# Kernel optimization log

Measured on AMD Instinct MI355X. Metric: run time of the kernel, lower is better.

The kernel has to match this reference:

```python
import jax, jax.numpy as jnp
import numpy as np

B, S, D = 2, 2048, 1024
H, DH = 16, 64
LN_EPS = 1e-5
NEG_INF = -1e9


def setup_inputs() -> dict:
    key = jax.random.key(0)
    ks = jax.random.split(key, 8)
    x = jax.random.normal(ks[0], (B, S, D), dtype=jnp.float32)
    mask = jax.random.randint(ks[1], (B, 1, S, S), 0, 5) == 0
    sc = 1.0 / np.sqrt(D)
    W_attn = jax.random.normal(ks[2], (D, 3 * H * DH), dtype=jnp.float32) * sc
    b_attn = jnp.zeros((3 * H * DH,), dtype=jnp.float32)
    W_out = jax.random.normal(ks[3], (H * DH, D), dtype=jnp.float32) * sc
    b_out = jnp.zeros((D,), dtype=jnp.float32)
    ln_g = jnp.ones((D,), dtype=jnp.float32)
    ln_b = jnp.zeros((D,), dtype=jnp.float32)
    return {"x": x, "W_attn": W_attn, "b_attn": b_attn, "W_out": W_out,
            "b_out": b_out, "ln_g": ln_g, "ln_b": ln_b, "mask": mask}


def reference(x, W_attn, b_attn, W_out, b_out, ln_g, ln_b, mask):
    bs, s, _ = x.shape
    qkv = x @ W_attn + b_attn                      # [b, s, 3*H*DH]
    q, k, v = jnp.split(qkv, 3, axis=-1)
    q = q.reshape(bs, s, H, DH)
    k = k.reshape(bs, s, H, DH)
    v = v.reshape(bs, s, H, DH)
    scores = jnp.einsum('bqhd,bkhd->bhqk', q, k) / np.sqrt(DH)
    scores = jnp.where(mask, NEG_INF, scores)
    probs = jax.nn.softmax(scores, axis=-1)        # attn_p = 0 -> dropout is identity
    attn = jnp.einsum('bhqk,bkhd->bqhd', probs, v).reshape(bs, s, H * DH)
    y = x + (attn @ W_out + b_out)                 # resid_p = 0
    mu = jnp.mean(y, axis=-1, keepdims=True)
    var = jnp.mean((y - mu) ** 2, axis=-1, keepdims=True)
    return (y - mu) * jax.lax.rsqrt(var + LN_EPS) * ln_g + ln_b
```

## Files before the change

kernel.cpp:

```cpp
#include <hip/hip_runtime.h>
#include <math.h>

#define BB 2
#define SS 2048
#define DD 1024
#define HH 16
#define DHD 64
#define N3 3072
#define LN_EPS 1e-5f

#define PLANE (BB*HH*SS*DHD)

typedef __attribute__((ext_vector_type(8))) short bf16x8;
typedef __attribute__((ext_vector_type(4))) float f32x4;
typedef __attribute__((ext_vector_type(16))) float f32x16;
typedef unsigned int u32;
typedef unsigned short ushort_t;

static __device__ __forceinline__ short f2bf(float f) {
  union { float f; unsigned u; } a;
  a.f = f;
  unsigned r = a.u + 0x7fffu + ((a.u >> 16) & 1u);
  return (short)(r >> 16);
}

static __device__ __forceinline__ u32 fbits(float f) {
  union { float f; u32 u; } a; a.f = f; return a.u;
}

static __device__ __forceinline__ float ex2(float x) {
  float r;
  asm("v_exp_f32 %0, %1" : "=v"(r) : "v"(x));
  return r;
}

static __device__ __forceinline__ u32 pkbf(float lo, float hi) {
  return __builtin_amdgcn_perm(fbits(hi) + 0x8000u, fbits(lo) + 0x8000u,
                               0x07060302u);
}

static __device__ __forceinline__ void gload_lds16(const void* g, void* l) {
  __builtin_amdgcn_global_load_lds(
      (const __attribute__((address_space(1))) u32*)g,
      (__attribute__((address_space(3))) u32*)l, 16, 0, 0);
}

#define PREP_CONV_B   2048
#define PREP_TA_B     768
#define PREP_TO_B     256
#define PREP_PACK_B   32768
#define PREP_TOTAL_B  (PREP_CONV_B + PREP_TA_B + PREP_TO_B + PREP_PACK_B)

__global__ __launch_bounds__(256) void prep_kernel(
    const float* __restrict__ x, ushort_t* __restrict__ xb,
    const float* __restrict__ Wa, ushort_t* __restrict__ watt,
    const float* __restrict__ Wo, ushort_t* __restrict__ wot,
    const int* __restrict__ mask, unsigned long long* __restrict__ bits) {
  __shared__ float tile[64][65];
  const int tid = threadIdx.x;
  const int bid = blockIdx.x;

  if (bid < PREP_CONV_B) {
    int i = (bid * 256 + tid) * 8;
    float4 a = *(const float4*)&x[i];
    float4 b = *(const float4*)&x[i + 4];
    short s[8] = {f2bf(a.x), f2bf(a.y), f2bf(a.z), f2bf(a.w),
                  f2bf(b.x), f2bf(b.y), f2bf(b.z), f2bf(b.w)};
    *(bf16x8*)&xb[i] = *(bf16x8*)s;
    return;
  }
  if (bid < PREP_CONV_B + PREP_TA_B + PREP_TO_B) {
    const float* W; ushort_t* Wt; int K, N, nb, kb;
    if (bid < PREP_CONV_B + PREP_TA_B) {
      int idx = bid - PREP_CONV_B;
      W = Wa; Wt = watt; K = DD; N = N3;
      nb = (idx % 48) * 64; kb = (idx / 48) * 64;
    } else {
      int idx = bid - PREP_CONV_B - PREP_TA_B;
      W = Wo; Wt = wot; K = DD; N = DD;
      nb = (idx % 16) * 64; kb = (idx / 16) * 64;
    }
    #pragma unroll
    for (int i = 0; i < 4; ++i) {
      int idx = tid + i * 256;
      int r = idx >> 4, c = (idx & 15) * 4;
      float4 v = *(const float4*)&W[(size_t)(kb + r) * N + nb + c];
      tile[r][c] = v.x; tile[r][c + 1] = v.y;
      tile[r][c + 2] = v.z; tile[r][c + 3] = v.w;
    }
    __syncthreads();
    #pragma unroll
    for (int i = 0; i < 4; ++i) {
      int idx = tid + i * 256;
      int n = idx >> 4, k = (idx & 15) * 4;
      short4 s;
      s.x = f2bf(tile[k][n]); s.y = f2bf(tile[k + 1][n]);
      s.z = f2bf(tile[k + 2][n]); s.w = f2bf(tile[k + 3][n]);
      *(short4*)&Wt[(size_t)(nb + n) * K + kb + k] = s;
    }
    return;
  }
  {
    size_t g = (size_t)(bid - PREP_CONV_B - PREP_TA_B - PREP_TO_B) * 256 + tid;
    int m = mask[g];
    unsigned long long b = __ballot(m != 0);
    if ((tid & 63) == 0) bits[g >> 6] = b;
  }
}

#define GEMM_MAIN(Aptr, Btptr, Kdim)                                          \
  __shared__ ushort_t As[128 * 64];                                           \
  __shared__ ushort_t Bs[128 * 64];                                           \
  const int tid = threadIdx.x;                                                \
  const int wave = tid >> 6, lane = tid & 63;                                 \
  const int lane16 = lane & 15, quad = lane >> 4;                             \
  const int wm = wave & 1, wn = wave >> 1;                                    \
  const int bm = blockIdx.y * 128, bn = blockIdx.x * 128;                     \
  const int srow = lane >> 3;                                                 \
  const int sg = (lane & 7) ^ srow;                                           \
  f32x4 acc[4][4];                                                            \
  _Pragma("unroll") for (int i = 0; i < 4; ++i)                               \
    _Pragma("unroll") for (int j = 0; j < 4; ++j)                             \
      acc[i][j] = (f32x4){0.f, 0.f, 0.f, 0.f};                                \
  const ushort_t* agp[4];                                                     \
  const ushort_t* bgp[4];                                                     \
  _Pragma("unroll") for (int i = 0; i < 4; ++i) {                             \
    int seg = wave * 4 + i;                                                   \
    int r = seg * 8 + srow;                                                   \
    agp[i] = Aptr + (size_t)(bm + r) * Kdim + sg * 8;                         \
    bgp[i] = Btptr + (size_t)(bn + r) * Kdim + sg * 8;                        \
  }                                                                           \
  for (int k0 = 0; k0 < Kdim; k0 += 64) {                                     \
    _Pragma("unroll") for (int i = 0; i < 4; ++i) {                           \
      int seg = wave * 4 + i;                                                 \
      gload_lds16(agp[i] + k0, &As[seg * 512]);                               \
      gload_lds16(bgp[i] + k0, &Bs[seg * 512]);                               \
    }                                                                         \
    __syncthreads();                                                          \
    _Pragma("unroll") for (int ks = 0; ks < 2; ++ks) {                        \
      bf16x8 af[4], bfr[4];                                                   \
      _Pragma("unroll") for (int mt = 0; mt < 4; ++mt) {                      \
        int ra = wm * 64 + mt * 16 + lane16;                                  \
        int kc = ks * 4 + quad;                                               \
        af[mt] = *(const bf16x8*)&As[ra * 64 + ((kc ^ (ra & 7)) * 8)];        \
      }                                                                       \
      _Pragma("unroll") for (int nt = 0; nt < 4; ++nt) {                      \
        int rb = wn * 64 + nt * 16 + lane16;                                  \
        int kc = ks * 4 + quad;                                               \
        bfr[nt] = *(const bf16x8*)&Bs[rb * 64 + ((kc ^ (rb & 7)) * 8)];       \
      }                                                                       \
      _Pragma("unroll") for (int mt = 0; mt < 4; ++mt)                        \
        _Pragma("unroll") for (int nt = 0; nt < 4; ++nt)                      \
          acc[mt][nt] = __builtin_amdgcn_mfma_f32_16x16x32_bf16(              \
              af[mt], bfr[nt], acc[mt][nt], 0, 0, 0);                         \
    }                                                                         \
    __syncthreads();                                                          \
  }

__global__ __launch_bounds__(256) void gemm_qkv_mfma(
    const ushort_t* __restrict__ A, const ushort_t* __restrict__ Bt,
    const float* __restrict__ bias, ushort_t* __restrict__ qkvh,
    ushort_t* __restrict__ vtb) {
  GEMM_MAIN(A, Bt, DD)
  #pragma unroll
  for (int nt = 0; nt < 4; ++nt) {
    int col = bn + wn * 64 + nt * 16 + lane16;
    int which = col >> 10, hcol = col & 1023;
    int head = hcol >> 6, d = hcol & 63;
    float bv = bias[col];
    if (which == 2) {
      #pragma unroll
      for (int mt = 0; mt < 4; ++mt) {
        #pragma unroll
        for (int reg = 0; reg < 4; ++reg) {
          int row = bm + wm * 64 + mt * 16 + quad * 4 + reg;
          int bb = row >> 11, ss = row & (SS - 1);
          vtb[((size_t)(bb * HH + head) * DHD + d) * SS + ss] =
              (ushort_t)f2bf(acc[mt][nt][reg] + bv);
        }
      }
    } else {
      ushort_t* plane = qkvh + (size_t)which * PLANE;
      #pragma unroll
      for (int mt = 0; mt < 4; ++mt) {
        #pragma unroll
        for (int reg = 0; reg < 4; ++reg) {
          int row = bm + wm * 64 + mt * 16 + quad * 4 + reg;
          int bb = row >> 11, ss = row & (SS - 1);
          plane[((size_t)(bb * HH + head) * SS + ss) * DHD + d] =
              (ushort_t)f2bf(acc[mt][nt][reg] + bv);
        }
      }
    }
  }
}

__global__ __launch_bounds__(256) void gemm_proj_mfma(
    const ushort_t* __restrict__ A, const ushort_t* __restrict__ Bt,
    const float* __restrict__ bias, const float* __restrict__ xres,
    float* __restrict__ Y) {
  GEMM_MAIN(A, Bt, DD)
  #pragma unroll
  for (int nt = 0; nt < 4; ++nt) {
    int col = bn + wn * 64 + nt * 16 + lane16;
    float bv = bias[col];
    #pragma unroll
    for (int mt = 0; mt < 4; ++mt) {
      #pragma unroll
      for (int reg = 0; reg < 4; ++reg) {
        int row = bm + wm * 64 + mt * 16 + quad * 4 + reg;
        Y[(size_t)row * DD + col] =
            acc[mt][nt][reg] + bv + xres[(size_t)row * DD + col];
      }
    }
  }
}

__global__ __launch_bounds__(512, 4) void attn_mfma_kernel(
    const ushort_t* __restrict__ qh, const ushort_t* __restrict__ kh,
    const ushort_t* __restrict__ vt, const u32* __restrict__ mbits,
    ushort_t* __restrict__ attn_out) {
  __shared__ __align__(16) ushort_t S[2][2][2][4096];

  const int tid = threadIdx.x;
  const int wave = tid >> 6, lane = tid & 63;
  const int l31 = lane & 31, hi = lane >> 5;

  const int bh = blockIdx.x & 31;
  const int qt = blockIdx.x >> 5;
  const int bbi = bh >> 4, hhi = bh & 15;
  const size_t head_base = (size_t)bh * SS * DHD;
  const int wq = wave & 3, khx = wave >> 2;
  const int q32 = qt * 128 + wq * 32;
  const int qrow = q32 + l31;

  bf16x8 qf[4];
  {
    const float kScale = 0.125f * 1.44269504f;
    const ushort_t* qsrc = &qh[head_base + (size_t)qrow * DHD + hi * 8];
    #pragma unroll
    for (int dk = 0; dk < 4; ++dk) {
      bf16x8 r = *(const bf16x8*)&qsrc[dk * 16];
      #pragma unroll
      for (int e = 0; e < 8; ++e) {
        union { u32 u; float f; } c;
        c.u = ((u32)(ushort_t)r[e]) << 16;
        c.f *= kScale;
        r[e] = f2bf(c.f);
      }
      qf[dk] = r;
    }
  }

  f32x16 acc0, acc1;
  #pragma unroll
  for (int e = 0; e < 16; ++e) { acc0[e] = 0.f; acc1[e] = 0.f; }
  float lsum = 0.f;

  const u32* mrow = mbits + ((size_t)(bbi * SS) + qrow) * 64 + khx * 32;

  const int sr = tid >> 3;
  const int scsrc = (tid & 7) ^ (sr & 7);
  const ushort_t* kst0 = kh + head_base + (size_t)sr * DHD + scsrc * 8;
  const ushort_t* vst0 = vt + head_base + (size_t)sr * SS + scsrc * 8;
  const int sdst = wave * 512;

#define ATTN_STAGE(buf, t)                                                    \
  gload_lds16(kst0 + (size_t)(t) * 64 * DHD, &S[buf][0][0][sdst]);            \
  gload_lds16(kst0 + (size_t)(1024 + (t) * 64) * DHD, &S[buf][0][1][sdst]);   \
  gload_lds16(vst0 + (t) * 64, &S[buf][1][0][sdst]);                          \
  gload_lds16(vst0 + 1024 + (t) * 64, &S[buf][1][1][sdst]);

  ATTN_STAGE(0, 0);
  uint2 mcur = *(const uint2*)mrow;
  __syncthreads();

  const int NT = 16;
  for (int t = 0; t < NT; ++t) {
    const int cur = t & 1;
    uint2 mnext = mcur;
    if (t + 1 < NT) {
      ATTN_STAGE(cur ^ 1, t + 1);
      mnext = *(const uint2*)&mrow[(t + 1) * 2];
    }

    const ushort_t* Kb = &S[cur][0][khx][0];
    const ushort_t* Vb = &S[cur][1][khx][0];

    f32x16 s0, s1;
    #pragma unroll
    for (int e = 0; e < 16; ++e) { s0[e] = 0.f; s1[e] = 0.f; }
    #pragma unroll
    for (int dk = 0; dk < 4; ++dk) {
      const int c = 2 * dk + hi;
      const int r0 = l31;
      bf16x8 kf0 = *(const bf16x8*)&Kb[r0 * 64 + ((c ^ (r0 & 7)) * 8)];
      s0 = __builtin_amdgcn_mfma_f32_32x32x16_bf16(kf0, qf[dk], s0, 0, 0, 0);
      const int r1 = 32 + l31;
      bf16x8 kf1 = *(const bf16x8*)&Kb[r1 * 64 + ((c ^ (r1 & 7)) * 8)];
      s1 = __builtin_amdgcn_mfma_f32_32x32x16_bf16(kf1, qf[dk], s1, 0, 0, 0);
    }

    #pragma unroll
    for (int ks16 = 0; ks16 < 4; ++ks16) {
      const int ksub = ks16 >> 1;
      const int g0 = (ks16 & 1) * 2;
      const f32x16 sv = ksub ? s1 : s0;
      const u32 w32 = ksub ? mcur.y : mcur.x;
      const u32 na = w32 >> (g0 * 8 + hi * 4);
      const u32 nb = w32 >> (g0 * 8 + 8 + hi * 4);
      float e0 = (na & 1u) ? 0.f : ex2(sv[g0 * 4 + 0]);
      float e1 = (na & 2u) ? 0.f : ex2(sv[g0 * 4 + 1]);
      float e2 = (na & 4u) ? 0.f : ex2(sv[g0 * 4 + 2]);
      float e3 = (na & 8u) ? 0.f : ex2(sv[g0 * 4 + 3]);
      float f0 = (nb & 1u) ? 0.f : ex2(sv[g0 * 4 + 4]);
      float f1 = (nb & 2u) ? 0.f : ex2(sv[g0 * 4 + 5]);
      float f2 = (nb & 4u) ? 0.f : ex2(sv[g0 * 4 + 6]);
      float f3 = (nb & 8u) ? 0.f : ex2(sv[g0 * 4 + 7]);
      lsum += ((e0 + e1) + (e2 + e3)) + ((f0 + f1) + (f2 + f3));
      u32 a0 = pkbf(e0, e1), a1 = pkbf(e2, e3);
      u32 b0 = pkbf(f0, f1), b1 = pkbf(f2, f3);
      asm("v_permlane32_swap_b32 %0, %1" : "+v"(a0), "+v"(b0));
      asm("v_permlane32_swap_b32 %0, %1" : "+v"(a1), "+v"(b1));
      union { u32 w[4]; bf16x8 v; } pfu;
      pfu.w[0] = a0; pfu.w[1] = a1; pfu.w[2] = b0; pfu.w[3] = b1;
      {
        const int rv0 = l31;
        const int cv = 2 * ks16 + hi;
        bf16x8 vf0 = *(const bf16x8*)&Vb[rv0 * 64 + ((cv ^ (rv0 & 7)) * 8)];
        acc0 = __builtin_amdgcn_mfma_f32_32x32x16_bf16(pfu.v, vf0, acc0, 0, 0, 0);
        const int rv1 = 32 + l31;
        bf16x8 vf1 = *(const bf16x8*)&Vb[rv1 * 64 + ((cv ^ (rv1 & 7)) * 8)];
        acc1 = __builtin_amdgcn_mfma_f32_32x32x16_bf16(pfu.v, vf1, acc1, 0, 0, 0);
      }
    }

    mcur = mnext;
    __syncthreads();
  }
#undef ATTN_STAGE

  float* mbuf = (float*)&S[0][0][0][0];
  float* lbuf = mbuf + 4 * 64 * 33;
  lbuf[((khx * 4 + wq) * 2 + hi) * 32 + l31] = lsum;
  if (khx == 1) {
    float* dst = mbuf + (size_t)(wq * 64 + lane) * 33;
    #pragma unroll
    for (int e = 0; e < 16; ++e) { dst[e] = acc0[e]; dst[16 + e] = acc1[e]; }
  }
  __syncthreads();
  if (khx == 0) {
    const float* src = mbuf + (size_t)(wq * 64 + lane) * 33;
    #pragma unroll
    for (int e = 0; e < 16; ++e) { acc0[e] += src[e]; acc1[e] += src[16 + e]; }
    #pragma unroll
    for (int reg = 0; reg < 16; ++reg) {
      const int kq = (reg & 3) + 8 * (reg >> 2) + 4 * hi;
      float lq = lbuf[((0 * 4 + wq) * 2 + 0) * 32 + kq]
               + lbuf[((0 * 4 + wq) * 2 + 1) * 32 + kq]
               + lbuf[((1 * 4 + wq) * 2 + 0) * 32 + kq]
               + lbuf[((1 * 4 + wq) * 2 + 1) * 32 + kq];
      const float inv = 1.0f / lq;
      ushort_t* orow = &attn_out[((size_t)(bbi * SS) + q32 + kq) * DD
                                 + hhi * DHD];
      orow[l31] = (ushort_t)f2bf(acc0[reg] * inv);
      orow[32 + l31] = (ushort_t)f2bf(acc1[reg] * inv);
    }
  }
}

__global__ __launch_bounds__(256) void ln_kernel(
    float* __restrict__ Y, const float* __restrict__ g,
    const float* __restrict__ bta) {
  const int r = blockIdx.x;
  const int tid = threadIdx.x;
  float4 v = *(const float4*)&Y[(size_t)r * DD + tid * 4];
  float sum = v.x + v.y + v.z + v.w;
  float sq = v.x * v.x + v.y * v.y + v.z * v.z + v.w * v.w;
  #pragma unroll
  for (int off = 32; off; off >>= 1) {
    sum += __shfl_down(sum, off);
    sq += __shfl_down(sq, off);
  }
  __shared__ float ps[4], pq[4];
  __shared__ float mu_s, rs_s;
  const int wave = tid >> 6;
  if ((tid & 63) == 0) { ps[wave] = sum; pq[wave] = sq; }
  __syncthreads();
  if (tid == 0) {
    float s = ps[0] + ps[1] + ps[2] + ps[3];
    float qq = pq[0] + pq[1] + pq[2] + pq[3];
    float mu = s * (1.0f / DD);
    float var = qq * (1.0f / DD) - mu * mu;
    mu_s = mu;
    rs_s = rsqrtf(var + LN_EPS);
  }
  __syncthreads();
  const float mu = mu_s, rs = rs_s;
  float4 g4 = *(const float4*)&g[tid * 4];
  float4 b4 = *(const float4*)&bta[tid * 4];
  float4 ov;
  ov.x = (v.x - mu) * rs * g4.x + b4.x;
  ov.y = (v.y - mu) * rs * g4.y + b4.y;
  ov.z = (v.z - mu) * rs * g4.z + b4.z;
  ov.w = (v.w - mu) * rs * g4.w + b4.w;
  *(float4*)&Y[(size_t)r * DD + tid * 4] = ov;
}

extern "C" void kernel_launch(void* const* d_in, const int* in_sizes, int n_in,
                              void* d_out, int out_size, void* d_ws, size_t ws_size,
                              hipStream_t stream) {
  const float* x      = (const float*)d_in[0];
  const float* W_attn = (const float*)d_in[1];
  const float* b_attn = (const float*)d_in[2];
  const float* W_out  = (const float*)d_in[3];
  const float* b_out  = (const float*)d_in[4];
  const float* ln_g   = (const float*)d_in[5];
  const float* ln_b   = (const float*)d_in[6];
  const int*   mask   = (const int*)d_in[7];
  float* out = (float*)d_out;
  ushort_t* ws = (ushort_t*)d_ws;

  ushort_t* xb    = ws;
  ushort_t* watt  = xb + (size_t)BB * SS * DD;
  ushort_t* wot   = watt + (size_t)N3 * DD;
  ushort_t* qh    = wot + (size_t)DD * DD;
  ushort_t* kh    = qh + (size_t)PLANE;
  ushort_t* vtb   = kh + (size_t)PLANE;
  ushort_t* attnb = vtb + (size_t)PLANE;
  u32* mbits      = (u32*)(attnb + (size_t)BB * SS * DD);

  prep_kernel<<<dim3(PREP_TOTAL_B), 256, 0, stream>>>(
      x, xb, W_attn, watt, W_out, wot, mask, (unsigned long long*)mbits);

  gemm_qkv_mfma<<<dim3(N3 / 128, (BB * SS) / 128), 256, 0, stream>>>(
      xb, watt, b_attn, qh, vtb);
  attn_mfma_kernel<<<dim3(BB * HH * (SS / 128)), 512, 0, stream>>>(
      qh, kh, vtb, mbits, attnb);
  gemm_proj_mfma<<<dim3(DD / 128, (BB * SS) / 128), 256, 0, stream>>>(
      attnb, wot, b_out, x, out);
  ln_kernel<<<dim3(BB * SS), 256, 0, stream>>>(out, ln_g, ln_b);
}
```

Baseline: 233.3 us.

## Compute softmax row sums via MFMA with ones and use hardware bf16 pack

The attention kernel drops the per-lane scalar row-sum accumulation and instead gets the softmax denominators from an extra MFMA that multiplies the probability fragment by a ones vector. It also swaps the manual perm-based bf16 packing for v_cvt_pk_bf16_f32, folds the zero-init of the score accumulators into the first MFMA, and raises wave priority around MFMA sections. This moves VALU adds and the LDS reduction of sums onto the matrix units, at the cost of one more MFMA per step and more accumulator registers. Row sums now come from bf16-rounded probabilities rather than fp32 values.

```diff
diff --git a/kernel.cpp b/kernel.cpp
--- a/kernel.cpp
+++ b/kernel.cpp
@@ -34,9 +34,10 @@
   return r;
 }
 
-static __device__ __forceinline__ u32 pkbf(float lo, float hi) {
-  return __builtin_amdgcn_perm(fbits(hi) + 0x8000u, fbits(lo) + 0x8000u,
-                               0x07060302u);
+static __device__ __forceinline__ u32 cvtpk(float lo, float hi) {
+  u32 r;
+  asm("v_cvt_pk_bf16_f32 %0, %1, %2" : "=v"(r) : "v"(lo), "v"(hi));
+  return r;
 }
 
 static __device__ __forceinline__ void gload_lds16(const void* g, void* l) {
@@ -252,10 +253,16 @@
     }
   }
 
-  f32x16 acc0, acc1;
-  #pragma unroll
-  for (int e = 0; e < 16; ++e) { acc0[e] = 0.f; acc1[e] = 0.f; }
-  float lsum = 0.f;
+  f32x16 zz;
+  #pragma unroll
+  for (int e = 0; e < 16; ++e) zz[e] = 0.f;
+  bf16x8 onesf;
+  #pragma unroll
+  for (int e = 0; e < 8; ++e) onesf[e] = (short)0x3F80;
+
+  f32x16 acc0, acc1, lacc;
+  #pragma unroll
+  for (int e = 0; e < 16; ++e) { acc0[e] = 0.f; acc1[e] = 0.f; lacc[e] = 0.f; }
 
   const u32* mrow = mbits + ((size_t)(bbi * SS) + qrow) * 64 + khx * 32;
 
@@ -288,18 +295,20 @@
     const ushort_t* Vb = &S[cur][1][khx][0];
 
     f32x16 s0, s1;
-    #pragma unroll
-    for (int e = 0; e < 16; ++e) { s0[e] = 0.f; s1[e] = 0.f; }
+    __builtin_amdgcn_s_setprio(1);
     #pragma unroll
     for (int dk = 0; dk < 4; ++dk) {
       const int c = 2 * dk + hi;
       const int r0 = l31;
       bf16x8 kf0 = *(const bf16x8*)&Kb[r0 * 64 + ((c ^ (r0 & 7)) * 8)];
-      s0 = __builtin_amdgcn_mfma_f32_32x32x16_bf16(kf0, qf[dk], s0, 0, 0, 0);
+      s0 = __builtin_amdgcn_mfma_f32_32x32x16_bf16(kf0, qf[dk],
+                                                   dk == 0 ? zz : s0, 0, 0, 0);
       const int r1 = 32 + l31;
       bf16x8 kf1 = *(const bf16x8*)&Kb[r1 * 64 + ((c ^ (r1 & 7)) * 8)];
-      s1 = __builtin_amdgcn_mfma_f32_32x32x16_bf16(kf1, qf[dk], s1, 0, 0, 0);
-    }
+      s1 = __builtin_amdgcn_mfma_f32_32x32x16_bf16(kf1, qf[dk],
+                                                   dk == 0 ? zz : s1, 0, 0, 0);
+    }
+    __builtin_amdgcn_s_setprio(0);
 
     #pragma unroll
     for (int ks16 = 0; ks16 < 4; ++ks16) {
@@ -317,9 +326,8 @@
       float f1 = (nb & 2u) ? 0.f : ex2(sv[g0 * 4 + 5]);
       float f2 = (nb & 4u) ? 0.f : ex2(sv[g0 * 4 + 6]);
       float f3 = (nb & 8u) ? 0.f : ex2(sv[g0 * 4 + 7]);
-      lsum += ((e0 + e1) + (e2 + e3)) + ((f0 + f1) + (f2 + f3));
-      u32 a0 = pkbf(e0, e1), a1 = pkbf(e2, e3);
-      u32 b0 = pkbf(f0, f1), b1 = pkbf(f2, f3);
+      u32 a0 = cvtpk(e0, e1), a1 = cvtpk(e2, e3);
+      u32 b0 = cvtpk(f0, f1), b1 = cvtpk(f2, f3);
       asm("v_permlane32_swap_b32 %0, %1" : "+v"(a0), "+v"(b0));
       asm("v_permlane32_swap_b32 %0, %1" : "+v"(a1), "+v"(b1));
       union { u32 w[4]; bf16x8 v; } pfu;
@@ -327,11 +335,14 @@
       {
         const int rv0 = l31;
         const int cv = 2 * ks16 + hi;
+        __builtin_amdgcn_s_setprio(1);
         bf16x8 vf0 = *(const bf16x8*)&Vb[rv0 * 64 + ((cv ^ (rv0 & 7)) * 8)];
         acc0 = __builtin_amdgcn_mfma_f32_32x32x16_bf16(pfu.v, vf0, acc0, 0, 0, 0);
         const int rv1 = 32 + l31;
         bf16x8 vf1 = *(const bf16x8*)&Vb[rv1 * 64 + ((cv ^ (rv1 & 7)) * 8)];
         acc1 = __builtin_amdgcn_mfma_f32_32x32x16_bf16(pfu.v, vf1, acc1, 0, 0, 0);
+        lacc = __builtin_amdgcn_mfma_f32_32x32x16_bf16(pfu.v, onesf, lacc, 0, 0, 0);
+        __builtin_amdgcn_s_setprio(0);
       }
     }
 
@@ -341,26 +352,24 @@
 #undef ATTN_STAGE
 
   float* mbuf = (float*)&S[0][0][0][0];
-  float* lbuf = mbuf + 4 * 64 * 33;
-  lbuf[((khx * 4 + wq) * 2 + hi) * 32 + l31] = lsum;
   if (khx == 1) {
-    float* dst = mbuf + (size_t)(wq * 64 + lane) * 33;
-    #pragma unroll
-    for (int e = 0; e < 16; ++e) { dst[e] = acc0[e]; dst[16 + e] = acc1[e]; }
+    float* dst = mbuf + (size_t)(wq * 64 + lane) * 49;
+    #pragma unroll
+    for (int e = 0; e < 16; ++e) {
+      dst[e] = acc0[e]; dst[16 + e] = acc1[e]; dst[32 + e] = lacc[e];
+    }
   }
   __syncthreads();
   if (khx == 0) {
-    const float* src = mbuf + (size_t)(wq * 64 + lane) * 33;
-    #pragma unroll
-    for (int e = 0; e < 16; ++e) { acc0[e] += src[e]; acc1[e] += src[16 + e]; }
+    const float* src = mbuf + (size_t)(wq * 64 + lane) * 49;
+    #pragma unroll
+    for (int e = 0; e < 16; ++e) {
+      acc0[e] += src[e]; acc1[e] += src[16 + e]; lacc[e] += src[32 + e];
+    }
     #pragma unroll
     for (int reg = 0; reg < 16; ++reg) {
       const int kq = (reg & 3) + 8 * (reg >> 2) + 4 * hi;
-      float lq = lbuf[((0 * 4 + wq) * 2 + 0) * 32 + kq]
-               + lbuf[((0 * 4 + wq) * 2 + 1) * 32 + kq]
-               + lbuf[((1 * 4 + wq) * 2 + 0) * 32 + kq]
-               + lbuf[((1 * 4 + wq) * 2 + 1) * 32 + kq];
-      const float inv = 1.0f / lq;
+      const float inv = 1.0f / lacc[reg];
       ushort_t* orow = &attn_out[((size_t)(bbi * SS) + q32 + kq) * DD
                                  + hhi * DHD];
       orow[l31] = (ushort_t)f2bf(acc0[reg] * inv);
```

Measured after the change: 240.5 us. +3.1%, slower.
